# Optimization experiments

Hardware: AMD Instinct MI355X
Metric: run time of the kernel (lower is better)

The kernel has to match this reference:

```python
import jax, jax.numpy as jnp
import numpy as np

B, N, IN_DIM, D, H, L = 4, 2048, 1, 256, 8, 4
DH = D // H          # 32 head dim
ROPE_D = DH // 2     # 16 = rotary dim per spatial axis (relative_emb_dim=2)
MIN_FREQ_SCALE = 64.0  # scale / min_freq = 1.0 / (1/64)
EPS = 1e-5


def setup_inputs():
    key = jax.random.key(0)
    ks = jax.random.split(key, 12)
    s = 0.02
    return {
        'h': jax.random.normal(ks[0], (B, N, IN_DIM), jnp.float32),
        'pos': jax.random.uniform(ks[1], (B, N, 2), jnp.float32),
        'proj_w': jax.random.normal(ks[2], (IN_DIM, D), jnp.float32) * s,
        'proj_b': jnp.zeros((D,), jnp.float32),
        'qkv_w': jax.random.normal(ks[3], (L, D, 3 * D), jnp.float32) * s,
        'out_w': jax.random.normal(ks[4], (L, D, D), jnp.float32) * s,
        'out_b': jnp.zeros((L, D), jnp.float32),
        'O_w': jax.random.normal(ks[5], (L, D, D), jnp.float32) * s,
        'O_b': jnp.zeros((L, D), jnp.float32),
        'ffn1_w': jax.random.normal(ks[6], (L, D, 2 * D), jnp.float32) * s,
        'ffn1_b': jnp.zeros((L, 2 * D), jnp.float32),
        'ffn2_w': jax.random.normal(ks[7], (L, 2 * D, D), jnp.float32) * s,
        'ffn2_b': jnp.zeros((L, D), jnp.float32),
        'ln1_g': jnp.ones((L, D), jnp.float32),
        'ln1_b': jnp.zeros((L, D), jnp.float32),
        'ln2_g': jnp.ones((L, D), jnp.float32),
        'ln2_b': jnp.zeros((L, D), jnp.float32),
        'final_w': jax.random.normal(ks[8], (D, D), jnp.float32) * s,
    }


def _rope_freqs(coords):
    # coords: (B, N) -> freqs (B, N, ROPE_D)
    inv_freq = 1.0 / (10000.0 ** (jnp.arange(0, ROPE_D, 2, dtype=jnp.float32) / ROPE_D))
    f = (coords * MIN_FREQ_SCALE)[..., None] * inv_freq
    return jnp.concatenate([f, f], axis=-1)


def _rotate_half(x):
    d = x.shape[-1] // 2
    return jnp.concatenate([-x[..., d:], x[..., :d]], axis=-1)


def _apply_rope(t, f):
    return t * jnp.cos(f) + _rotate_half(t) * jnp.sin(f)


def _apply_2d_rope(t, ft, fx):
    d = t.shape[-1] // 2
    return jnp.concatenate([_apply_rope(t[..., :d], ft), _apply_rope(t[..., d:], fx)], axis=-1)


def _ln(x, g, b):
    m = jnp.mean(x, -1, keepdims=True)
    v = jnp.mean((x - m) ** 2, -1, keepdims=True)
    return (x - m) / jnp.sqrt(v + EPS) * g + b


def _forward(h, pos, proj_w, proj_b, qkv_w, out_w, out_b, O_w, O_b,
             ffn1_w, ffn1_b, ffn2_w, ffn2_b, ln1_g, ln1_b, ln2_g, ln2_b, final_w):
    h = h @ proj_w + proj_b                      # (B, N, D)
    ft = _rope_freqs(pos[..., 0])[:, None]       # (B, 1, N, ROPE_D) broadcast over heads
    fx = _rope_freqs(pos[..., 1])[:, None]
    scale = DH ** -0.5
    for l in range(L):
        qkv = h @ qkv_w[l]                       # (B, N, 3D)
        q, k, v = jnp.split(qkv, 3, axis=-1)
        to_heads = lambda t: t.reshape(B, N, H, DH).transpose(0, 2, 1, 3)
        q, k, v = to_heads(q), to_heads(k), to_heads(v)
        q = _apply_2d_rope(q, ft, fx)
        k = _apply_2d_rope(k, ft, fx)
        attn = jax.nn.softmax(jnp.einsum('bhid,bhjd->bhij', q, k) * scale, axis=-1)
        o = jnp.einsum('bhij,bhjd->bhid', attn, v)
        o = o.transpose(0, 2, 1, 3).reshape(B, N, D)
        o = o @ out_w[l] + out_b[l]              # attention to_out
        o = o @ O_w[l] + O_b[l]                  # layer O projection
        h = _ln(h + o, ln1_g[l], ln1_b[l])
        f = jax.nn.relu(h @ ffn1_w[l] + ffn1_b[l]) @ ffn2_w[l] + ffn2_b[l]
        h = _ln(h + f, ln2_g[l], ln2_b[l])
    return h @ final_w


def reference(h, pos, proj_w, proj_b, qkv_w, out_w, out_b, O_w, O_b,
              ffn1_w, ffn1_b, ffn2_w, ffn2_b, ln1_g, ln1_b, ln2_g, ln2_b, final_w):
    return _forward(h, pos, proj_w, proj_b, qkv_w, out_w, out_b, O_w, O_b,
                    ffn1_w, ffn1_b, ffn2_w, ffn2_b, ln1_g, ln1_b, ln2_g, ln2_b, final_w)
```

## Files before the change

kernel.cpp:

```cpp
#include <hip/hip_runtime.h>
#include <math.h>

#define B_ 4
#define N_ 2048
#define D_ 256
#define H_ 8
#define L_ 4
#define DH_ 32

typedef float f32x4 __attribute__((ext_vector_type(4)));
typedef float f32x16 __attribute__((ext_vector_type(16)));
typedef short short8 __attribute__((ext_vector_type(8)));
typedef unsigned short ushort_t;
typedef ushort_t ushortx4 __attribute__((ext_vector_type(4)));
typedef ushort_t ushortx8 __attribute__((ext_vector_type(8)));

typedef __attribute__((address_space(3))) unsigned int lds_u32_t;
typedef __attribute__((address_space(1))) unsigned int glb_u32_t;

static __device__ __forceinline__ ushort_t f2bf(float x) {
    unsigned int u = __float_as_uint(x);
    unsigned int r = (u + 0x7fffu + ((u >> 16) & 1u)) >> 16;
    return (ushort_t)r;
}

static __device__ __forceinline__ unsigned int cvt_pk_bf16(float a, float b) {
    unsigned int w;
    asm("v_cvt_pk_bf16_f32 %0, %1, %2" : "=v"(w) : "v"(a), "v"(b));
    return w;
}

__global__ __launch_bounds__(256) void proj_kernel(
    const float* __restrict__ hin, const float* __restrict__ w,
    const float* __restrict__ bias, float* __restrict__ hout,
    ushort_t* __restrict__ hb)
{
    long idx = (long)blockIdx.x * 256 + threadIdx.x;
    long bn = idx >> 6;
    int d4 = (int)(idx & 63) << 2;
    float hv = hin[bn];
    float4 wv = *(const float4*)&w[d4];
    float4 bv = *(const float4*)&bias[d4];
    float4 o;
    o.x = hv * wv.x + bv.x;
    o.y = hv * wv.y + bv.y;
    o.z = hv * wv.z + bv.z;
    o.w = hv * wv.w + bv.w;
    *(float4*)&hout[bn * D_ + d4] = o;
    ushortx4 ob;
    ob[0] = f2bf(o.x); ob[1] = f2bf(o.y); ob[2] = f2bf(o.z); ob[3] = f2bf(o.w);
    *(ushortx4*)&hb[bn * D_ + d4] = ob;
}

__global__ __launch_bounds__(256) void rope_table_kernel(
    const float* __restrict__ pos, float* __restrict__ tab)
{
    int i = blockIdx.x * 256 + threadIdx.x;
    if (i >= B_ * N_) return;
    float t = pos[i * 2 + 0] * 64.0f;
    float x = pos[i * 2 + 1] * 64.0f;
    float* o = tab + (long)i * 32;
    const float log2_1e4_over8 = 13.28771237954945f / 8.0f;
    #pragma unroll
    for (int j = 0; j < 8; ++j) {
        float invf = exp2f(-(float)j * log2_1e4_over8);
        float st, ct, sx, cx;
        sincosf(t * invf, &st, &ct);
        sincosf(x * invf, &sx, &cx);
        o[j]      = ct;
        o[8 + j]  = st;
        o[16 + j] = cx;
        o[24 + j] = sx;
    }
}

__global__ __launch_bounds__(256) void rope_convert_kernel(
    const float* __restrict__ qkv, const float* __restrict__ tab,
    ushort_t* __restrict__ Qb, ushort_t* __restrict__ Kb)
{
    const float F = 0.17677669529663687f * 1.4426950408889634f;
    long idx = (long)blockIdx.x * 256 + threadIdx.x;
    int p = (int)(idx & 15);
    int h = (int)((idx >> 4) & 7);
    long bn = idx >> 7;
    int half = p >> 3;
    int j = p & 7;
    const float* tb = tab + bn * 32;
    float c = tb[half * 16 + j];
    float s = tb[half * 16 + 8 + j];
    float cF = c * F, sF = s * F;
    int b = (int)(bn >> 11);
    int n = (int)(bn & 2047);
    long obase = ((long)(b * H_ + h) * N_ + n) * DH_;
    const float* base = qkv + bn * (3 * D_) + h * DH_ + half * 16 + j;
    int d0 = half * 16 + j;
    float q0 = base[0], q1 = base[8];
    Qb[obase + d0]     = f2bf(q0 * cF - q1 * sF);
    Qb[obase + d0 + 8] = f2bf(q1 * cF + q0 * sF);
    float k0 = base[D_], k1 = base[D_ + 8];
    Kb[obase + d0]     = f2bf(k0 * c - k1 * s);
    Kb[obase + d0 + 8] = f2bf(k1 * c + k0 * s);
}

__global__ __launch_bounds__(256) void vtrans_kernel(
    const float* __restrict__ qkv, ushort_t* __restrict__ Vt)
{
    int bh = blockIdx.y;
    int b = bh >> 3, h = bh & 7;
    int n0 = blockIdx.x << 6;
    __shared__ float T[64][36];
    int t = threadIdx.x;
    int r = t >> 2, c0 = (t & 3) << 3;
    const float* src = qkv + ((long)b * N_ + n0 + r) * (3 * D_) + 2 * D_ + h * DH_ + c0;
    float4 a = ((const float4*)src)[0];
    float4 bb = ((const float4*)src)[1];
    *(float4*)&T[r][c0] = a;
    *(float4*)&T[r][c0 + 4] = bb;
    __syncthreads();
    int d = t >> 3, n8 = (t & 7) << 3;
    ushortx8 o;
    #pragma unroll
    for (int i = 0; i < 8; ++i) o[i] = f2bf(T[n8 + i][d]);
    *(ushortx8*)&Vt[((long)bh * DH_ + d) * N_ + n0 + n8] = o;
}

__global__ __launch_bounds__(256) void wprep_kernel(
    const float* __restrict__ qkv_w, const float* __restrict__ out_w,
    const float* __restrict__ O_w, const float* __restrict__ ffn1_w,
    const float* __restrict__ ffn2_w, const float* __restrict__ final_w,
    ushort_t* __restrict__ WT)
{
    int bid = blockIdx.x;
    const float* src; ushort_t* dst; int K, Nn, tile;
    if (bid < 192)      { int l = bid / 48;        tile = bid % 48;        src = qkv_w  + (long)l * 196608; dst = WT + (long)l * 196608;           K = 256; Nn = 768; }
    else if (bid < 256) { int r = bid - 192; int l = r / 16; tile = r % 16; src = out_w  + (long)l * 65536;  dst = WT + 786432  + (long)l * 65536;  K = 256; Nn = 256; }
    else if (bid < 320) { int r = bid - 256; int l = r / 16; tile = r % 16; src = O_w    + (long)l * 65536;  dst = WT + 1048576 + (long)l * 65536;  K = 256; Nn = 256; }
    else if (bid < 448) { int r = bid - 320; int l = r / 32; tile = r % 32; src = ffn1_w + (long)l * 131072; dst = WT + 1310720 + (long)l * 131072; K = 256; Nn = 512; }
    else if (bid < 576) { int r = bid - 448; int l = r / 32; tile = r % 32; src = ffn2_w + (long)l * 131072; dst = WT + 1835008 + (long)l * 131072; K = 512; Nn = 256; }
    else                { tile = bid - 576;                                 src = final_w;                   dst = WT + 2359296;                    K = 256; Nn = 256; }
    int ntn = Nn >> 6;
    int kt = (tile / ntn) << 6;
    int nt = (tile % ntn) << 6;
    __shared__ float Tl[64][65];
    int t = threadIdx.x;
    int kr = t >> 2, nc0 = (t & 3) << 4;
    const float* sp = src + (long)(kt + kr) * Nn + nt + nc0;
    float4 v0 = ((const float4*)sp)[0];
    float4 v1 = ((const float4*)sp)[1];
    float4 v2 = ((const float4*)sp)[2];
    float4 v3 = ((const float4*)sp)[3];
    float* tr = &Tl[kr][nc0];
    tr[0] = v0.x; tr[1] = v0.y; tr[2] = v0.z; tr[3] = v0.w;
    tr[4] = v1.x; tr[5] = v1.y; tr[6] = v1.z; tr[7] = v1.w;
    tr[8] = v2.x; tr[9] = v2.y; tr[10] = v2.z; tr[11] = v2.w;
    tr[12] = v3.x; tr[13] = v3.y; tr[14] = v3.z; tr[15] = v3.w;
    __syncthreads();
    int n = t >> 2, kc0 = (t & 3) << 4;
    ushortx8 o0, o1;
    #pragma unroll
    for (int i = 0; i < 8; ++i) o0[i] = f2bf(Tl[kc0 + i][n]);
    #pragma unroll
    for (int i = 0; i < 8; ++i) o1[i] = f2bf(Tl[kc0 + 8 + i][n]);
    ushort_t* dp = dst + (long)(nt + n) * K + kt + kc0;
    *(ushortx8*)dp = o0;
    *(ushortx8*)(dp + 8) = o1;
}

__global__ __launch_bounds__(256) void wfold_kernel(
    const float* __restrict__ out_w, const float* __restrict__ O_w,
    ushort_t* __restrict__ WTp)
{
    int l = blockIdx.x >> 4;
    int t4 = blockIdx.x & 15;
    int k0 = (t4 >> 2) << 6, n0 = (t4 & 3) << 6;
    const float* Am = out_w + (long)l * 65536;
    const float* Bm = O_w + (long)l * 65536;
    ushort_t* dst = WTp + (long)l * 65536;
    __shared__ float sA[16][68];
    __shared__ float sB[16][64];
    int tid = threadIdx.x;
    int tx = tid & 15, ty = tid >> 4;
    int arow = tid >> 2, acol = (tid & 3) << 2;
    int brow = tid >> 4, bcol = (tid & 15) << 2;
    const float* Aptr = Am + (long)(k0 + arow) * 256 + acol;
    const float* Bptr = Bm + (long)brow * 256 + n0 + bcol;
    float acc[4][4] = {{0.f}};
    for (int jt = 0; jt < 256; jt += 16) {
        float4 av = *(const float4*)(Aptr + jt);
        float4 bv = *(const float4*)(Bptr + (long)jt * 256);
        __syncthreads();
        sA[acol + 0][arow] = av.x;
        sA[acol + 1][arow] = av.y;
        sA[acol + 2][arow] = av.z;
        sA[acol + 3][arow] = av.w;
        *(float4*)&sB[brow][bcol] = bv;
        __syncthreads();
        #pragma unroll
        for (int kk = 0; kk < 16; ++kk) {
            float4 a = *(const float4*)&sA[kk][ty << 2];
            float4 b = *(const float4*)&sB[kk][tx << 2];
            acc[0][0] += a.x * b.x; acc[0][1] += a.x * b.y; acc[0][2] += a.x * b.z; acc[0][3] += a.x * b.w;
            acc[1][0] += a.y * b.x; acc[1][1] += a.y * b.y; acc[1][2] += a.y * b.z; acc[1][3] += a.y * b.w;
            acc[2][0] += a.z * b.x; acc[2][1] += a.z * b.y; acc[2][2] += a.z * b.z; acc[2][3] += a.z * b.w;
            acc[3][0] += a.w * b.x; acc[3][1] += a.w * b.y; acc[3][2] += a.w * b.z; acc[3][3] += a.w * b.w;
        }
    }
    #pragma unroll
    for (int i = 0; i < 4; ++i) {
        int k = k0 + (ty << 2) + i;
        #pragma unroll
        for (int c = 0; c < 4; ++c) {
            int n = n0 + (tx << 2) + c;
            dst[(long)n * 256 + k] = f2bf(acc[i][c]);
        }
    }
}

__global__ __launch_bounds__(256) void bfold_kernel(
    const float* __restrict__ out_b, const float* __restrict__ O_w,
    const float* __restrict__ O_b, float* __restrict__ bp)
{
    int l = blockIdx.x >> 3;
    int n = ((blockIdx.x & 7) << 5) + (threadIdx.x & 31);
    int jg = threadIdx.x >> 5;
    const float* Bm = O_w + (long)l * 65536;
    float acc = 0.f;
    #pragma unroll 8
    for (int j = jg * 32; j < jg * 32 + 32; ++j)
        acc += out_b[l * 256 + j] * Bm[(long)j * 256 + n];
    __shared__ float red[8][32];
    red[jg][threadIdx.x & 31] = acc;
    __syncthreads();
    if (threadIdx.x < 32) {
        int nn = ((blockIdx.x & 7) << 5) + threadIdx.x;
        float s = O_b[l * 256 + nn];
        #pragma unroll
        for (int g = 0; g < 8; ++g) s += red[g][threadIdx.x];
        bp[l * 256 + nn] = s;
    }
}

__global__ __launch_bounds__(256) void gemm_mfma2(
    const ushort_t* __restrict__ A, const ushort_t* __restrict__ BT,
    const float* __restrict__ bias, void* __restrict__ Cout,
    int N, int K, int flags)
{
    __shared__ ushort_t sA[2][8192];
    __shared__ ushort_t sB[2][4096];
    int tid = threadIdx.x;
    int wid = tid >> 6, lane = tid & 63;
    int lo = lane & 15, hi = lane >> 4;
    int wm = wid >> 1, wn = wid & 1;
    int m0 = blockIdx.y << 7, n0 = blockIdx.x << 6;

    int lrow = lane >> 3;
    int slot = lane & 7;
    const ushort_t* Ag[4];
    const ushort_t* Bg[2];
    #pragma unroll
    for (int c = 0; c < 4; ++c) {
        int arow = (wid << 5) + (c << 3) + lrow;
        Ag[c] = A + (long)(m0 + arow) * K + ((slot ^ lrow) << 3);
    }
    #pragma unroll
    for (int c = 0; c < 2; ++c) {
        int brow = (wid << 4) + (c << 3) + lrow;
        Bg[c] = BT + (long)(n0 + brow) * K + ((slot ^ lrow) << 3);
    }

#define STAGE(buf, koff) do { \
    _Pragma("unroll") \
    for (int c = 0; c < 4; ++c) \
        __builtin_amdgcn_global_load_lds((const glb_u32_t*)(Ag[c] + (koff)), \
            (lds_u32_t*)&sA[buf][((wid << 5) + (c << 3)) << 6], 16, 0, 0); \
    _Pragma("unroll") \
    for (int c = 0; c < 2; ++c) \
        __builtin_amdgcn_global_load_lds((const glb_u32_t*)(Bg[c] + (koff)), \
            (lds_u32_t*)&sB[buf][((wid << 4) + (c << 3)) << 6], 16, 0, 0); \
} while (0)

    f32x4 acc[4][2];
    #pragma unroll
    for (int i = 0; i < 4; ++i)
        #pragma unroll
        for (int j = 0; j < 2; ++j) acc[i][j] = (f32x4){0.f, 0.f, 0.f, 0.f};

    int ar[4], br[2];
    #pragma unroll
    for (int mf = 0; mf < 4; ++mf) ar[mf] = ((wm << 6) + (mf << 4) + lo) << 6;
    #pragma unroll
    for (int nf = 0; nf < 2; ++nf) br[nf] = ((wn << 5) + (nf << 4) + lo) << 6;
    int swz = lo & 7;

    int nk = K >> 6;
    STAGE(0, 0);
    for (int s = 0; s < nk; ++s) {
        int buf = s & 1;
        if (s + 1 < nk) {
            STAGE(buf ^ 1, (s + 1) << 6);
            asm volatile("s_waitcnt vmcnt(6)" ::: "memory");
        } else {
            asm volatile("s_waitcnt vmcnt(0)" ::: "memory");
        }
        __builtin_amdgcn_s_barrier();
        asm volatile("" ::: "memory");
        #pragma unroll
        for (int ks = 0; ks < 2; ++ks) {
            int ko = (((ks << 2) + hi) ^ swz) << 3;
            short8 a0 = *(const short8*)&sA[buf][ar[0] + ko];
            short8 a1 = *(const short8*)&sA[buf][ar[1] + ko];
            short8 a2 = *(const short8*)&sA[buf][ar[2] + ko];
            short8 a3 = *(const short8*)&sA[buf][ar[3] + ko];
            short8 b0 = *(const short8*)&sB[buf][br[0] + ko];
            short8 b1 = *(const short8*)&sB[buf][br[1] + ko];
            acc[0][0] = __builtin_amdgcn_mfma_f32_16x16x32_bf16(a0, b0, acc[0][0], 0, 0, 0);
            acc[0][1] = __builtin_amdgcn_mfma_f32_16x16x32_bf16(a0, b1, acc[0][1], 0, 0, 0);
            acc[1][0] = __builtin_amdgcn_mfma_f32_16x16x32_bf16(a1, b0, acc[1][0], 0, 0, 0);
            acc[1][1] = __builtin_amdgcn_mfma_f32_16x16x32_bf16(a1, b1, acc[1][1], 0, 0, 0);
            acc[2][0] = __builtin_amdgcn_mfma_f32_16x16x32_bf16(a2, b0, acc[2][0], 0, 0, 0);
            acc[2][1] = __builtin_amdgcn_mfma_f32_16x16x32_bf16(a2, b1, acc[2][1], 0, 0, 0);
            acc[3][0] = __builtin_amdgcn_mfma_f32_16x16x32_bf16(a3, b0, acc[3][0], 0, 0, 0);
            acc[3][1] = __builtin_amdgcn_mfma_f32_16x16x32_bf16(a3, b1, acc[3][1], 0, 0, 0);
        }
        asm volatile("" ::: "memory");
        __builtin_amdgcn_s_barrier();
    }
#undef STAGE

    #pragma unroll
    for (int nf = 0; nf < 2; ++nf) {
        int col = n0 + (wn << 5) + (nf << 4) + lo;
        float bv = (flags & 1) ? bias[col] : 0.f;
        #pragma unroll
        for (int mf = 0; mf < 4; ++mf) {
            #pragma unroll
            for (int j = 0; j < 4; ++j) {
                float v = acc[mf][nf][j] + bv;
                if (flags & 2) v = fmaxf(v, 0.f);
                long row = m0 + (wm << 6) + (mf << 4) + (hi << 2) + j;
                if (flags & 4) ((ushort_t*)Cout)[row * N + col] = f2bf(v);
                else           ((float*)Cout)[row * N + col] = v;
            }
        }
    }
}

__global__ __launch_bounds__(256) void attn_mfma4(
    const ushort_t* __restrict__ Qb, const ushort_t* __restrict__ Kb,
    const ushort_t* __restrict__ Vt, ushort_t* __restrict__ o)
{
    int bh = blockIdx.y;
    int tid = threadIdx.x;
    int wid = tid >> 6, lane = tid & 63;
    int lq = lane & 31;
    int half = lane >> 5;
    int qbase = (blockIdx.x << 7) + wid * 32;

    const ushort_t* Qp = Qb + (long)bh * N_ * DH_;
    const ushort_t* kp = Kb + (long)bh * N_ * DH_ + lq * DH_ + half * 8;
    const ushort_t* vp = Vt + (long)bh * DH_ * N_ + (long)lq * N_ + half * 8;

    short8 qf0 = *(const short8*)&Qp[(long)(qbase + lq) * DH_ + half * 8];
    short8 qf1 = *(const short8*)&Qp[(long)(qbase + lq) * DH_ + 16 + half * 8];

    f32x16 acc;
    #pragma unroll
    for (int r = 0; r < 16; ++r) acc[r] = 0.f;
    float m = -1e30f, lsum = 0.f;

    short8 k00 = *(const short8*)(kp +  0 * DH_);
    short8 k01 = *(const short8*)(kp +  0 * DH_ + 16);
    short8 k10 = *(const short8*)(kp + 32 * DH_);
    short8 k11 = *(const short8*)(kp + 32 * DH_ + 16);
    short8 v00 = *(const short8*)(vp +  0);
    short8 v01 = *(const short8*)(vp + 16);
    short8 v10 = *(const short8*)(vp + 32);
    short8 v11 = *(const short8*)(vp + 48);

#define ATTN_TILE(K00, K01, K10, K11, V00, V01, V10, V11) do {                  \
    f32x16 sa, sb;                                                              \
    _Pragma("unroll")                                                           \
    for (int r = 0; r < 16; ++r) { sa[r] = 0.f; sb[r] = 0.f; }                  \
    sa = __builtin_amdgcn_mfma_f32_32x32x16_bf16(K00, qf0, sa, 0, 0, 0);        \
    sa = __builtin_amdgcn_mfma_f32_32x32x16_bf16(K01, qf1, sa, 0, 0, 0);        \
    sb = __builtin_amdgcn_mfma_f32_32x32x16_bf16(K10, qf0, sb, 0, 0, 0);        \
    sb = __builtin_amdgcn_mfma_f32_32x32x16_bf16(K11, qf1, sb, 0, 0, 0);        \
    float pmax = fmaxf(sa[0], sb[0]);                                           \
    _Pragma("unroll")                                                           \
    for (int r = 1; r < 16; ++r) pmax = fmaxf(pmax, fmaxf(sa[r], sb[r]));       \
    pmax = fmaxf(pmax, __shfl_xor(pmax, 32, 64));                               \
    if (!__all(pmax <= m + 8.f)) {                                              \
        float mn = fmaxf(m, pmax);                                              \
        float corr = __builtin_amdgcn_exp2f(m - mn);                            \
        m = mn; lsum *= corr;                                                   \
        _Pragma("unroll")                                                       \
        for (int r = 0; r < 16; ++r) {                                          \
            int qr = (r & 3) + 8 * (r >> 2) + 4 * half;                         \
            acc[r] *= __shfl(corr, qr, 64);                                     \
        }                                                                       \
    }                                                                           \
    float sum = 0.f;                                                            \
    _Pragma("unroll")                                                           \
    for (int r = 0; r < 16; ++r) {                                              \
        sa[r] = __builtin_amdgcn_exp2f(sa[r] - m); sum += sa[r];                \
        sb[r] = __builtin_amdgcn_exp2f(sb[r] - m); sum += sb[r];                \
    }                                                                           \
    sum += __shfl_xor(sum, 32, 64);                                             \
    lsum += sum;                                                                \
    unsigned int a0 = cvt_pk_bf16(sa[0], sa[1]),   a1 = cvt_pk_bf16(sa[2], sa[3]);   \
    unsigned int a2 = cvt_pk_bf16(sa[4], sa[5]),   a3 = cvt_pk_bf16(sa[6], sa[7]);   \
    unsigned int a4 = cvt_pk_bf16(sa[8], sa[9]),   a5 = cvt_pk_bf16(sa[10], sa[11]); \
    unsigned int a6 = cvt_pk_bf16(sa[12], sa[13]), a7 = cvt_pk_bf16(sa[14], sa[15]); \
    unsigned int b0 = cvt_pk_bf16(sb[0], sb[1]),   b1 = cvt_pk_bf16(sb[2], sb[3]);   \
    unsigned int b2 = cvt_pk_bf16(sb[4], sb[5]),   b3 = cvt_pk_bf16(sb[6], sb[7]);   \
    unsigned int b4 = cvt_pk_bf16(sb[8], sb[9]),   b5 = cvt_pk_bf16(sb[10], sb[11]); \
    unsigned int b6 = cvt_pk_bf16(sb[12], sb[13]), b7 = cvt_pk_bf16(sb[14], sb[15]); \
    asm volatile("v_permlane32_swap_b32 %0, %1" : "+v"(a0), "+v"(a2));          \
    asm volatile("v_permlane32_swap_b32 %0, %1" : "+v"(a1), "+v"(a3));          \
    asm volatile("v_permlane32_swap_b32 %0, %1" : "+v"(a4), "+v"(a6));          \
    asm volatile("v_permlane32_swap_b32 %0, %1" : "+v"(a5), "+v"(a7));          \
    asm volatile("v_permlane32_swap_b32 %0, %1" : "+v"(b0), "+v"(b2));          \
    asm volatile("v_permlane32_swap_b32 %0, %1" : "+v"(b1), "+v"(b3));          \
    asm volatile("v_permlane32_swap_b32 %0, %1" : "+v"(b4), "+v"(b6));          \
    asm volatile("v_permlane32_swap_b32 %0, %1" : "+v"(b5), "+v"(b7));          \
    union { unsigned int u[4]; short8 s8; } p0, p1, p2, p3;                     \
    p0.u[0] = a0; p0.u[1] = a1; p0.u[2] = a2; p0.u[3] = a3;                     \
    p1.u[0] = a4; p1.u[1] = a5; p1.u[2] = a6; p1.u[3] = a7;                     \
    p2.u[0] = b0; p2.u[1] = b1; p2.u[2] = b2; p2.u[3] = b3;                     \
    p3.u[0] = b4; p3.u[1] = b5; p3.u[2] = b6; p3.u[3] = b7;                     \
    acc = __builtin_amdgcn_mfma_f32_32x32x16_bf16(p0.s8, V00, acc, 0, 0, 0);    \
    acc = __builtin_amdgcn_mfma_f32_32x32x16_bf16(p1.s8, V01, acc, 0, 0, 0);    \
    acc = __builtin_amdgcn_mfma_f32_32x32x16_bf16(p2.s8, V10, acc, 0, 0, 0);    \
    acc = __builtin_amdgcn_mfma_f32_32x32x16_bf16(p3.s8, V11, acc, 0, 0, 0);    \
} while (0)

    for (int it = 0; it < N_ / 64 - 1; ++it) {
        long kn = (long)(it + 1) << 6;
        short8 nk00 = *(const short8*)(kp + (kn +  0) * DH_);
        short8 nk01 = *(const short8*)(kp + (kn +  0) * DH_ + 16);
        short8 nk10 = *(const short8*)(kp + (kn + 32) * DH_);
        short8 nk11 = *(const short8*)(kp + (kn + 32) * DH_ + 16);
        short8 nv00 = *(const short8*)(vp + kn);
        short8 nv01 = *(const short8*)(vp + kn + 16);
        short8 nv10 = *(const short8*)(vp + kn + 32);
        short8 nv11 = *(const short8*)(vp + kn + 48);
        ATTN_TILE(k00, k01, k10, k11, v00, v01, v10, v11);
        k00 = nk00; k01 = nk01; k10 = nk10; k11 = nk11;
        v00 = nv00; v01 = nv01; v10 = nv10; v11 = nv11;
    }
    ATTN_TILE(k00, k01, k10, k11, v00, v01, v10, v11);
#undef ATTN_TILE

    float invl = 1.f / lsum;
    int b = bh >> 3, h = bh & 7;
    #pragma unroll
    for (int r = 0; r < 16; ++r) {
        int qr = (r & 3) + 8 * (r >> 2) + 4 * half;
        float iv = __shfl(invl, qr, 64);
        long row = (long)b * N_ + qbase + qr;
        o[row * D_ + h * DH_ + lq] = f2bf(acc[r] * iv);
    }
}

__global__ __launch_bounds__(256) void add_ln_kernel(
    float* __restrict__ h, const float* __restrict__ r,
    const float* __restrict__ g, const float* __restrict__ be,
    ushort_t* __restrict__ hb)
{
    int row = blockIdx.x * 4 + (threadIdx.x >> 6);
    int lane = threadIdx.x & 63;
    long off = (long)row * D_ + (lane << 2);
    float4 x = *(float4*)&h[off];
    float4 rr = *(const float4*)&r[off];
    x.x += rr.x; x.y += rr.y; x.z += rr.z; x.w += rr.w;
    float s = x.x + x.y + x.z + x.w;
    #pragma unroll
    for (int k = 1; k < 64; k <<= 1) s += __shfl_xor(s, k, 64);
    float mean = s * (1.f / 256.f);
    float dx = x.x - mean, dy = x.y - mean, dz = x.z - mean, dw = x.w - mean;
    float sq = dx * dx + dy * dy + dz * dz + dw * dw;
    #pragma unroll
    for (int k = 1; k < 64; k <<= 1) sq += __shfl_xor(sq, k, 64);
    float rstd = rsqrtf(sq * (1.f / 256.f) + 1e-5f);
    float4 gv = *(const float4*)&g[lane << 2];
    float4 bv = *(const float4*)&be[lane << 2];
    float4 o;
    o.x = dx * rstd * gv.x + bv.x;
    o.y = dy * rstd * gv.y + bv.y;
    o.z = dz * rstd * gv.z + bv.z;
    o.w = dw * rstd * gv.w + bv.w;
    *(float4*)&h[off] = o;
    ushortx4 ob;
    ob[0] = f2bf(o.x); ob[1] = f2bf(o.y); ob[2] = f2bf(o.z); ob[3] = f2bf(o.w);
    *(ushortx4*)&hb[off] = ob;
}

extern "C" void kernel_launch(void* const* d_in, const int* in_sizes, int n_in,
                              void* d_out, int out_size, void* d_ws, size_t ws_size,
                              hipStream_t stream) {
    const float* h_in    = (const float*)d_in[0];
    const float* pos     = (const float*)d_in[1];
    const float* proj_w  = (const float*)d_in[2];
    const float* proj_b  = (const float*)d_in[3];
    const float* qkv_w   = (const float*)d_in[4];
    const float* out_w   = (const float*)d_in[5];
    const float* out_b   = (const float*)d_in[6];
    const float* O_w     = (const float*)d_in[7];
    const float* O_b     = (const float*)d_in[8];
    const float* ffn1_w  = (const float*)d_in[9];
    const float* ffn1_b  = (const float*)d_in[10];
    const float* ffn2_w  = (const float*)d_in[11];
    const float* ffn2_b  = (const float*)d_in[12];
    const float* ln1_g   = (const float*)d_in[13];
    const float* ln1_b   = (const float*)d_in[14];
    const float* ln2_g   = (const float*)d_in[15];
    const float* ln2_b   = (const float*)d_in[16];
    const float* final_w = (const float*)d_in[17];
    float* out = (float*)d_out;

    float* ws   = (float*)d_ws;
    float* h    = ws;
    float* hb_f = h + 2097152;
    float* tab  = hb_f + 1048576;
    float* WT_f = tab + 262144;
    float* R    = WT_f + 1212416;
    float* QKV  = R + 6291456;
    float* tf   = QKV + 3145728;

    ushort_t* hb  = (ushort_t*)hb_f;
    ushort_t* WT  = (ushort_t*)WT_f;
    float*    qkvf = R;
    ushort_t* aob = (ushort_t*)R;
    ushort_t* fb  = (ushort_t*)(R + 2097152);
    float*    tf32 = R + 4194304;
    ushort_t* Qb  = (ushort_t*)QKV;
    ushort_t* Kb  = Qb + 2097152;
    ushort_t* Vtg = Kb + 2097152;
    ushort_t* WTp = (ushort_t*)tf;
    float*    bp  = tf + 131072;

    const long qkvT_off  = 0;
    const long ffn1T_off = 1310720;
    const long ffn2T_off = 1835008;
    const long finT_off  = 2359296;

    const long M = (long)B_ * N_;

    wprep_kernel<<<592, 256, 0, stream>>>(qkv_w, out_w, O_w, ffn1_w, ffn2_w, final_w, WT);
    wfold_kernel<<<64, 256, 0, stream>>>(out_w, O_w, WTp);
    bfold_kernel<<<32, 256, 0, stream>>>(out_b, O_w, O_b, bp);
    proj_kernel<<<(M * 64) / 256, 256, 0, stream>>>(h_in, proj_w, proj_b, h, hb);
    rope_table_kernel<<<(B_ * N_) / 256, 256, 0, stream>>>(pos, tab);

    for (int l = 0; l < L_; ++l) {
        gemm_mfma2<<<dim3(768 / 64, M / 128), 256, 0, stream>>>(
            hb, WT + qkvT_off + (long)l * 196608, nullptr, qkvf, 768, 256, 0);
        rope_convert_kernel<<<(M * H_ * 16) / 256, 256, 0, stream>>>(qkvf, tab, Qb, Kb);
        vtrans_kernel<<<dim3(N_ / 64, B_ * H_), 256, 0, stream>>>(qkvf, Vtg);
        attn_mfma4<<<dim3(N_ / 128, B_ * H_), 256, 0, stream>>>(Qb, Kb, Vtg, aob);
        gemm_mfma2<<<dim3(256 / 64, M / 128), 256, 0, stream>>>(
            aob, WTp + (long)l * 65536, bp + (long)l * 256, tf32, 256, 256, 1);
        add_ln_kernel<<<M / 4, 256, 0, stream>>>(
            h, tf32, ln1_g + (long)l * D_, ln1_b + (long)l * D_, hb);
        gemm_mfma2<<<dim3(512 / 64, M / 128), 256, 0, stream>>>(
            hb, WT + ffn1T_off + (long)l * 131072, ffn1_b + (long)l * 2 * D_, fb, 512, 256, 1 | 2 | 4);
        gemm_mfma2<<<dim3(256 / 64, M / 128), 256, 0, stream>>>(
            fb, WT + ffn2T_off + (long)l * 131072, ffn2_b + (long)l * D_, tf32, 256, 512, 1);
        add_ln_kernel<<<M / 4, 256, 0, stream>>>(
            h, tf32, ln2_g + (long)l * D_, ln2_b + (long)l * D_, hb);
    }
    gemm_mfma2<<<dim3(256 / 64, M / 128), 256, 0, stream>>>(
        hb, WT + finT_off, nullptr, out, 256, 256, 0);
}
```

Measured before the change: 559.6 us.

## Split attention KV range across two blocks and fuse RoPE with V transpose

Attention now processes each query tile twice, each pass covering half the key/value sequence. Each pass writes unnormalized fp32 partial outputs plus a running max and sum, and a new combine kernel merges the two halves, normalises, and writes bf16. This doubles the number of attention blocks so the GPU has more work in flight per CU, at the cost of extra fp32 partial-result traffic and one more launch. Separately, the RoPE conversion of Q/K and the V transpose are merged into a single kernel, removing one launch and one separate pass over the QKV buffer.

```diff
diff --git a/kernel.cpp b/kernel.cpp
--- a/kernel.cpp
+++ b/kernel.cpp
@@ -74,42 +74,38 @@
     }
 }
 
-__global__ __launch_bounds__(256) void rope_convert_kernel(
+__global__ __launch_bounds__(256) void prep_qkv(
     const float* __restrict__ qkv, const float* __restrict__ tab,
-    ushort_t* __restrict__ Qb, ushort_t* __restrict__ Kb)
+    ushort_t* __restrict__ Qb, ushort_t* __restrict__ Kb, ushort_t* __restrict__ Vt)
 {
     const float F = 0.17677669529663687f * 1.4426950408889634f;
-    long idx = (long)blockIdx.x * 256 + threadIdx.x;
-    int p = (int)(idx & 15);
-    int h = (int)((idx >> 4) & 7);
-    long bn = idx >> 7;
-    int half = p >> 3;
-    int j = p & 7;
-    const float* tb = tab + bn * 32;
-    float c = tb[half * 16 + j];
-    float s = tb[half * 16 + 8 + j];
-    float cF = c * F, sF = s * F;
-    int b = (int)(bn >> 11);
-    int n = (int)(bn & 2047);
-    long obase = ((long)(b * H_ + h) * N_ + n) * DH_;
-    const float* base = qkv + bn * (3 * D_) + h * DH_ + half * 16 + j;
-    int d0 = half * 16 + j;
-    float q0 = base[0], q1 = base[8];
-    Qb[obase + d0]     = f2bf(q0 * cF - q1 * sF);
-    Qb[obase + d0 + 8] = f2bf(q1 * cF + q0 * sF);
-    float k0 = base[D_], k1 = base[D_ + 8];
-    Kb[obase + d0]     = f2bf(k0 * c - k1 * s);
-    Kb[obase + d0 + 8] = f2bf(k1 * c + k0 * s);
-}
-
-__global__ __launch_bounds__(256) void vtrans_kernel(
-    const float* __restrict__ qkv, ushort_t* __restrict__ Vt)
-{
     int bh = blockIdx.y;
     int b = bh >> 3, h = bh & 7;
     int n0 = blockIdx.x << 6;
+    int t = threadIdx.x;
+
+    #pragma unroll
+    for (int i = 0; i < 4; ++i) {
+        int item = t + (i << 8);
+        int tok = item >> 4, p = item & 15;
+        long bn = (long)b * N_ + n0 + tok;
+        int half = p >> 3, j = p & 7;
+        const float* tb = tab + bn * 32;
+        float c = tb[half * 16 + j];
+        float s = tb[half * 16 + 8 + j];
+        float cF = c * F, sF = s * F;
+        long obase = ((long)bh * N_ + n0 + tok) * DH_;
+        const float* base = qkv + bn * (3 * D_) + h * DH_ + half * 16 + j;
+        int d0 = half * 16 + j;
+        float q0 = base[0], q1 = base[8];
+        Qb[obase + d0]     = f2bf(q0 * cF - q1 * sF);
+        Qb[obase + d0 + 8] = f2bf(q1 * cF + q0 * sF);
+        float k0 = base[D_], k1 = base[D_ + 8];
+        Kb[obase + d0]     = f2bf(k0 * c - k1 * s);
+        Kb[obase + d0 + 8] = f2bf(k1 * c + k0 * s);
+    }
+
     __shared__ float T[64][36];
-    int t = threadIdx.x;
     int r = t >> 2, c0 = (t & 3) << 3;
     const float* src = qkv + ((long)b * N_ + n0 + r) * (3 * D_) + 2 * D_ + h * DH_ + c0;
     float4 a = ((const float4*)src)[0];
@@ -345,20 +341,22 @@
     }
 }
 
-__global__ __launch_bounds__(256) void attn_mfma4(
+__global__ __launch_bounds__(256) void attn_split(
     const ushort_t* __restrict__ Qb, const ushort_t* __restrict__ Kb,
-    const ushort_t* __restrict__ Vt, ushort_t* __restrict__ o)
+    const ushort_t* __restrict__ Vt, float* __restrict__ Op,
+    float2* __restrict__ ml)
 {
     int bh = blockIdx.y;
+    int qt = blockIdx.x & 15, sp = blockIdx.x >> 4;
     int tid = threadIdx.x;
     int wid = tid >> 6, lane = tid & 63;
     int lq = lane & 31;
     int half = lane >> 5;
-    int qbase = (blockIdx.x << 7) + wid * 32;
+    int qbase = (qt << 7) + wid * 32;
 
     const ushort_t* Qp = Qb + (long)bh * N_ * DH_;
-    const ushort_t* kp = Kb + (long)bh * N_ * DH_ + lq * DH_ + half * 8;
-    const ushort_t* vp = Vt + (long)bh * DH_ * N_ + (long)lq * N_ + half * 8;
+    const ushort_t* kp = Kb + (long)bh * N_ * DH_ + ((long)sp << 10) * DH_ + lq * DH_ + half * 8;
+    const ushort_t* vp = Vt + (long)bh * DH_ * N_ + (long)lq * N_ + (sp << 10) + half * 8;
 
     short8 qf0 = *(const short8*)&Qp[(long)(qbase + lq) * DH_ + half * 8];
     short8 qf1 = *(const short8*)&Qp[(long)(qbase + lq) * DH_ + 16 + half * 8];
@@ -434,7 +432,8 @@
     acc = __builtin_amdgcn_mfma_f32_32x32x16_bf16(p3.s8, V11, acc, 0, 0, 0);    \
 } while (0)
 
-    for (int it = 0; it < N_ / 64 - 1; ++it) {
+    const int NITER = 1024 / 64;
+    for (int it = 0; it < NITER - 1; ++it) {
         long kn = (long)(it + 1) << 6;
         short8 nk00 = *(const short8*)(kp + (kn +  0) * DH_);
         short8 nk01 = *(const short8*)(kp + (kn +  0) * DH_ + 16);
@@ -451,15 +450,49 @@
     ATTN_TILE(k00, k01, k10, k11, v00, v01, v10, v11);
 #undef ATTN_TILE
 
-    float invl = 1.f / lsum;
-    int b = bh >> 3, h = bh & 7;
+    float* OpB = Op + (long)sp * 2097152;
+    float2* mlB = ml + (long)sp * 65536;
     #pragma unroll
     for (int r = 0; r < 16; ++r) {
         int qr = (r & 3) + 8 * (r >> 2) + 4 * half;
-        float iv = __shfl(invl, qr, 64);
-        long row = (long)b * N_ + qbase + qr;
-        o[row * D_ + h * DH_ + lq] = f2bf(acc[r] * iv);
-    }
+        long row = (long)bh * N_ + qbase + qr;
+        OpB[row * 32 + lq] = acc[r];
+    }
+    if (lane < 32) mlB[(long)bh * N_ + qbase + lq] = make_float2(m, lsum);
+}
+
+__global__ __launch_bounds__(256) void attn_combine(
+    const float* __restrict__ Op, const float2* __restrict__ ml,
+    ushort_t* __restrict__ o)
+{
+    int i = blockIdx.x * 256 + threadIdx.x;
+    int bh = i >> 11, q = i & 2047;
+    int b = bh >> 3, h = bh & 7;
+    float2 m0 = ml[i];
+    float2 m1 = ml[65536 + i];
+    float mn = fmaxf(m0.x, m1.x);
+    float c0 = __builtin_amdgcn_exp2f(m0.x - mn);
+    float c1 = __builtin_amdgcn_exp2f(m1.x - mn);
+    float inv = 1.f / (c0 * m0.y + c1 * m1.y);
+    float f0 = c0 * inv, f1 = c1 * inv;
+    const f32x4* O0 = (const f32x4*)(Op + (long)i * 32);
+    const f32x4* O1 = (const f32x4*)(Op + 2097152 + (long)i * 32);
+    unsigned int w[16];
+    #pragma unroll
+    for (int v = 0; v < 8; ++v) {
+        f32x4 a = O0[v], bb = O1[v];
+        float e0 = f0 * a[0] + f1 * bb[0];
+        float e1 = f0 * a[1] + f1 * bb[1];
+        float e2 = f0 * a[2] + f1 * bb[2];
+        float e3 = f0 * a[3] + f1 * bb[3];
+        w[2 * v]     = cvt_pk_bf16(e0, e1);
+        w[2 * v + 1] = cvt_pk_bf16(e2, e3);
+    }
+    uint4* dst = (uint4*)&o[((long)b * N_ + q) * D_ + h * DH_];
+    dst[0] = make_uint4(w[0], w[1], w[2], w[3]);
+    dst[1] = make_uint4(w[4], w[5], w[6], w[7]);
+    dst[2] = make_uint4(w[8], w[9], w[10], w[11]);
+    dst[3] = make_uint4(w[12], w[13], w[14], w[15]);
 }
 
 __global__ __launch_bounds__(256) void add_ln_kernel(
@@ -531,6 +564,7 @@
     ushort_t* WT  = (ushort_t*)WT_f;
     float*    qkvf = R;
     ushort_t* aob = (ushort_t*)R;
+    float*    Op  = R + 2097152;
     ushort_t* fb  = (ushort_t*)(R + 2097152);
     float*    tf32 = R + 4194304;
     ushort_t* Qb  = (ushort_t*)QKV;
@@ -538,6 +572,7 @@
     ushort_t* Vtg = Kb + 2097152;
     ushort_t* WTp = (ushort_t*)tf;
     float*    bp  = tf + 131072;
+    float2*   mlb = (float2*)(tf + 262144);
 
     const long qkvT_off  = 0;
     const long ffn1T_off = 1310720;
@@ -555,9 +590,9 @@
     for (int l = 0; l < L_; ++l) {
         gemm_mfma2<<<dim3(768 / 64, M / 128), 256, 0, stream>>>(
             hb, WT + qkvT_off + (long)l * 196608, nullptr, qkvf, 768, 256, 0);
-        rope_convert_kernel<<<(M * H_ * 16) / 256, 256, 0, stream>>>(qkvf, tab, Qb, Kb);
-        vtrans_kernel<<<dim3(N_ / 64, B_ * H_), 256, 0, stream>>>(qkvf, Vtg);
-        attn_mfma4<<<dim3(N_ / 128, B_ * H_), 256, 0, stream>>>(Qb, Kb, Vtg, aob);
+        prep_qkv<<<dim3(N_ / 64, B_ * H_), 256, 0, stream>>>(qkvf, tab, Qb, Kb, Vtg);
+        attn_split<<<dim3(32, B_ * H_), 256, 0, stream>>>(Qb, Kb, Vtg, Op, mlb);
+        attn_combine<<<256, 256, 0, stream>>>(Op, mlb, aob);
         gemm_mfma2<<<dim3(256 / 64, M / 128), 256, 0, stream>>>(
             aob, WTp + (long)l * 65536, bp + (long)l * 256, tf32, 256, 256, 1);
         add_ln_kernel<<<M / 4, 256, 0, stream>>>(
```

After: 594.7 us. 1.06x slower.
